# Kernel optimization log

Measured on AMD Instinct MI355X. Metric: run time of the kernel, lower is better.

The kernel has to match this reference:

```python
import jax, jax.numpy as jnp
import numpy as np

B, N, D = 4, 2048, 1024
H = 16
HD = D // H


def setup_inputs() -> dict:
    key = jax.random.key(0)
    ks = jax.random.split(key, 6)
    x = jax.random.normal(ks[0], (B, N, D), dtype=jnp.float32)
    # additive causal mask: 0 on/below diagonal, -inf above
    neg = jnp.float32(-1e9)
    causal_mask = jnp.where(jnp.triu(jnp.ones((N, N), dtype=bool), k=1), neg, 0.0).astype(jnp.float32)
    s = 1.0 / np.sqrt(D)
    Wqkv = jax.random.normal(ks[1], (D, 3 * D), dtype=jnp.float32) * s
    bqkv = jax.random.normal(ks[2], (3 * D,), dtype=jnp.float32) * 0.01
    Wproj = jax.random.normal(ks[3], (D, D), dtype=jnp.float32) * s
    bproj = jax.random.normal(ks[4], (D,), dtype=jnp.float32) * 0.01
    return {"x": x, "causal_mask": causal_mask, "Wqkv": Wqkv, "bqkv": bqkv, "Wproj": Wproj, "bproj": bproj}


def reference(x, causal_mask, Wqkv, bqkv, Wproj, bproj):
    b, n, d = x.shape
    qkv = x @ Wqkv + bqkv  # [B,N,3D]
    qkv = qkv.reshape(b, n, 3, H, HD).transpose(2, 0, 3, 1, 4)  # [3,B,H,N,HD]
    q, k, v = qkv[0], qkv[1], qkv[2]
    scale = HD ** -0.5
    attn = jnp.einsum('bhqd,bhkd->bhqk', q, k) * scale  # [B,H,N,N]
    attn = attn + causal_mask  # broadcast [N,N] -> [B,H,N,N]
    attn = jax.nn.softmax(attn, axis=-1)
    out = jnp.einsum('bhqk,bhkd->bhqd', attn, v)  # [B,H,N,HD]
    out = out.transpose(0, 2, 1, 3).reshape(b, n, d)
    return out @ Wproj + bproj
```

## Files before the change

### kernel.cpp

```cpp
#include <hip/hip_runtime.h>
#include <hip/hip_bf16.h>

typedef unsigned short u16;
typedef unsigned int u32;
typedef __attribute__((ext_vector_type(8))) short bf16x8;
typedef __attribute__((ext_vector_type(4))) float f32x4;
typedef __attribute__((ext_vector_type(16))) float f32x16;

#define AS1(p) ((const __attribute__((address_space(1))) void*)(p))
#define AS3(p) ((__attribute__((address_space(3))) void*)(p))

#if __has_builtin(__builtin_amdgcn_exp2f)
#define EXP2F(x) __builtin_amdgcn_exp2f(x)
#else
#define EXP2F(x) exp2f(x)
#endif

static __device__ __forceinline__ float b2f(u16 u) {
  union { unsigned int i; float f; } v; v.i = ((unsigned int)u) << 16; return v.f;
}
static __device__ __forceinline__ u16 f2b(float f) {
  union { float f; unsigned int i; } v; v.f = f;
  unsigned int r = v.i + 0x7FFFu + ((v.i >> 16) & 1u);
  return (u16)(r >> 16);
}
static __device__ __forceinline__ u32 cvt_pk_bf16(float lo, float hi) {
  u32 r;
  asm("v_cvt_pk_bf16_f32 %0, %1, %2" : "=v"(r) : "v"(lo), "v"(hi));
  return r;
}
static __device__ __forceinline__ void permswap(u32& a, u32& b) {
  asm("v_permlane32_swap_b32 %0, %1" : "+v"(a), "+v"(b));
}

__global__ __launch_bounds__(256) void cast_f32_bf16(const float* __restrict__ src,
                                                     u16* __restrict__ dst, int n8) {
  int stride = gridDim.x * blockDim.x;
  for (int i = blockIdx.x * blockDim.x + threadIdx.x; i < n8; i += stride) {
    const float4* s = (const float4*)(src + (size_t)i * 8);
    float4 a = s[0], b = s[1];
    bf16x8 o;
    o[0] = (short)f2b(a.x); o[1] = (short)f2b(a.y); o[2] = (short)f2b(a.z); o[3] = (short)f2b(a.w);
    o[4] = (short)f2b(b.x); o[5] = (short)f2b(b.y); o[6] = (short)f2b(b.z); o[7] = (short)f2b(b.w);
    *(bf16x8*)(dst + (size_t)i * 8) = o;
  }
}

__global__ __launch_bounds__(256) void transpose_w(const float* __restrict__ src,
                                                   u16* __restrict__ dst,
                                                   int R, int C) {
  __shared__ float tile[32][33];
  int c0 = blockIdx.x * 32, r0 = blockIdx.y * 32;
  int tx = threadIdx.x, ty = threadIdx.y;
  for (int i = ty; i < 32; i += 8) tile[i][tx] = src[(size_t)(r0 + i) * C + c0 + tx];
  __syncthreads();
  for (int i = ty; i < 32; i += 8) dst[(size_t)(c0 + i) * R + r0 + tx] = f2b(tile[tx][i]);
}

__global__ __launch_bounds__(256) void transpose_v(const u16* __restrict__ qkv,
                                                   u16* __restrict__ VT) {
  const int N = 2048, TD = 3072, D = 1024;
  int bh = blockIdx.y, n0 = blockIdx.x * 64;
  int b = bh >> 4, h = bh & 15;
  int tid = threadIdx.x;
  __shared__ u16 tl[64][72];
  #pragma unroll
  for (int i = 0; i < 16; ++i) {
    int idx = tid + i * 256;
    int nl = idx >> 6, dd = idx & 63;
    tl[dd][nl] = qkv[(size_t)(b * N + n0 + nl) * TD + 2 * D + h * 64 + dd];
  }
  __syncthreads();
  #pragma unroll
  for (int i = 0; i < 16; ++i) {
    int idx = tid + i * 256;
    int dd = idx >> 6, nl = idx & 63;
    VT[((size_t)bh * 64 + dd) * N + n0 + nl] = tl[dd][nl];
  }
}

template <typename OutT>
__global__ __launch_bounds__(256) void gemm_bt_bias(
    const u16* __restrict__ A,
    const u16* __restrict__ BT,
    const float* __restrict__ bias,
    OutT* __restrict__ C,
    int M, int N, int K) {
  __shared__ alignas(16) u16 Als[128 * 32];
  __shared__ alignas(16) u16 Bls[128 * 32];
  const int m0 = blockIdx.x * 128, n0 = blockIdx.y * 128;
  const int t = threadIdx.x;
  const int w = t >> 6, lane = t & 63;
  const int wr = w >> 1, wc = w & 1;
  const int rlo = lane & 15, g = lane >> 4;

  f32x4 acc[4][4] = {};

  const int r0 = t >> 2;
  const int c0 = (t & 3) << 3;
  const u16* aSrc = A + (size_t)(m0 + r0) * K + c0;
  const u16* bSrc = BT + (size_t)(n0 + r0) * K + c0;

  for (int k0 = 0; k0 < K; k0 += 32) {
    __builtin_amdgcn_global_load_lds(AS1(aSrc + k0), AS3(&Als[t * 8]), 16, 0, 0);
    __builtin_amdgcn_global_load_lds(AS1(aSrc + (size_t)64 * K + k0), AS3(&Als[(t + 256) * 8]), 16, 0, 0);
    __builtin_amdgcn_global_load_lds(AS1(bSrc + k0), AS3(&Bls[t * 8]), 16, 0, 0);
    __builtin_amdgcn_global_load_lds(AS1(bSrc + (size_t)64 * K + k0), AS3(&Bls[(t + 256) * 8]), 16, 0, 0);
    __syncthreads();

    bf16x8 a[4], b[4];
    #pragma unroll
    for (int m = 0; m < 4; ++m)
      a[m] = *(const bf16x8*)&Als[(wr * 64 + m * 16 + rlo) * 32 + g * 8];
    #pragma unroll
    for (int n = 0; n < 4; ++n)
      b[n] = *(const bf16x8*)&Bls[(wc * 64 + n * 16 + rlo) * 32 + g * 8];
    #pragma unroll
    for (int m = 0; m < 4; ++m)
      #pragma unroll
      for (int n = 0; n < 4; ++n)
        acc[m][n] = __builtin_amdgcn_mfma_f32_16x16x32_bf16(a[m], b[n], acc[m][n], 0, 0, 0);
    __syncthreads();
  }

  #pragma unroll
  for (int n = 0; n < 4; ++n) {
    const int col = n0 + wc * 64 + n * 16 + rlo;
    const float bv = bias[col];
    #pragma unroll
    for (int m = 0; m < 4; ++m) {
      const int row = m0 + wr * 64 + m * 16 + g * 4;
      #pragma unroll
      for (int i = 0; i < 4; ++i) {
        float r = acc[m][n][i] + bv;
        if constexpr (sizeof(OutT) == 2)
          C[(size_t)(row + i) * N + col] = (OutT)f2b(r);
        else
          C[(size_t)(row + i) * N + col] = (OutT)r;
      }
    }
  }
}

__global__ __launch_bounds__(256) void attn_fwd(
    const u16* __restrict__ qkv,
    const u16* __restrict__ VT,
    u16* __restrict__ O) {
  const int N = 2048, TD = 3072, D = 1024;
  const int bid = blockIdx.x;
  const int qp = bid >> 6, bh = bid & 63;
  const int b = bh >> 4, h = bh & 15;
  const int t = threadIdx.x, w = t >> 6, lane = t & 63;
  const int l31 = lane & 31, hi = lane >> 5;

  __shared__ alignas(16) u16 Kls[64 * 64];
  __shared__ alignas(16) u16 Vls[64 * 64];

  const int c1 = t, c2 = t + 256;
  const int r1 = c1 >> 3, sc1 = ((c1 & 7) ^ (r1 & 7)) * 8;
  const int r2 = c2 >> 3, sc2 = ((c2 & 7) ^ (r2 & 7)) * 8;
  const u16* kbase = qkv + (size_t)(b * N) * TD + D + h * 64;
  const u16* vbase = VT + (size_t)bh * 64 * N;

  const float L2E = 1.44269504089f;
  const float NSH = -23.0830992f;

  for (int pass = 0; pass < 2; ++pass) {
    const int qt = pass ? (15 - qp) : qp;
    const int qbase = qt * 128 + w * 32;

    bf16x8 qf[4];
    {
      const u16* qp_ = qkv + ((size_t)(b * N) + qbase + l31) * TD + h * 64 + hi * 8;
      #pragma unroll
      for (int c = 0; c < 4; ++c) {
        bf16x8 v = *(const bf16x8*)(qp_ + c * 16);
        #pragma unroll
        for (int j = 0; j < 8; ++j)
          v[j] = (short)f2b(b2f((u16)v[j]) * 0.125f);
        qf[c] = v;
      }
    }

    f32x16 o_acc[2] = {};
    float psum = 0.f;
    const int jend = qt * 128 + 64;

    for (int j0 = 0; j0 <= jend; j0 += 64) {
      __builtin_amdgcn_global_load_lds(AS1(kbase + (size_t)(j0 + r1) * TD + sc1), AS3(&Kls[c1 * 8]), 16, 0, 0);
      __builtin_amdgcn_global_load_lds(AS1(kbase + (size_t)(j0 + r2) * TD + sc2), AS3(&Kls[c2 * 8]), 16, 0, 0);
      __builtin_amdgcn_global_load_lds(AS1(vbase + (size_t)r1 * N + j0 + sc1), AS3(&Vls[c1 * 8]), 16, 0, 0);
      __builtin_amdgcn_global_load_lds(AS1(vbase + (size_t)r2 * N + j0 + sc2), AS3(&Vls[c2 * 8]), 16, 0, 0);
      __syncthreads();

      if (j0 <= qbase + 31) {
        bf16x8 kf[2][4];
        #pragma unroll
        for (int st = 0; st < 2; ++st) {
          const int row = st * 32 + l31, sw = (row & 7) << 3;
          #pragma unroll
          for (int c = 0; c < 4; ++c)
            kf[st][c] = *(const bf16x8*)&Kls[row * 64 + ((c * 16 + hi * 8) ^ sw)];
        }
        bf16x8 vf[2][2][2];
        #pragma unroll
        for (int dt = 0; dt < 2; ++dt) {
          const int row = dt * 32 + l31, sw = (row & 7) << 3;
          #pragma unroll
          for (int st = 0; st < 2; ++st)
            #pragma unroll
            for (int kc = 0; kc < 2; ++kc)
              vf[st][kc][dt] = *(const bf16x8*)&Vls[row * 64 + ((st * 32 + kc * 16 + hi * 8) ^ sw)];
        }

        const int qr = qbase + l31;
        const bool straddle = !(j0 + 63 <= qbase);
        #pragma unroll
        for (int st = 0; st < 2; ++st) {
          if (st == 1 && !(j0 < qbase)) continue;
          f32x16 S = {};
          __builtin_amdgcn_s_setprio(1);
          #pragma unroll
          for (int c = 0; c < 4; ++c)
            S = __builtin_amdgcn_mfma_f32_32x32x16_bf16(kf[st][c], qf[c], S, 0, 0, 0);
          __builtin_amdgcn_s_setprio(0);
          if (straddle) {
            const int kvb = j0 + st * 32 + 4 * hi;
            #pragma unroll
            for (int r = 0; r < 16; ++r)
              if (kvb + (r & 3) + 8 * (r >> 2) > qr) S[r] = -1e30f;
          }
          float p[16];
          #pragma unroll
          for (int r = 0; r < 16; ++r) p[r] = EXP2F(fmaf(S[r], L2E, NSH));
          float ps = 0.f;
          #pragma unroll
          for (int r = 0; r < 16; ++r) ps += p[r];
          psum += ps;
          u32 wq[8];
          #pragma unroll
          for (int i = 0; i < 8; ++i) wq[i] = cvt_pk_bf16(p[2 * i], p[2 * i + 1]);
          permswap(wq[0], wq[2]); permswap(wq[1], wq[3]);
          permswap(wq[4], wq[6]); permswap(wq[5], wq[7]);
          union { u32 u[4]; bf16x8 v; } pa0, pa1;
          pa0.u[0] = wq[0]; pa0.u[1] = wq[1]; pa0.u[2] = wq[2]; pa0.u[3] = wq[3];
          pa1.u[0] = wq[4]; pa1.u[1] = wq[5]; pa1.u[2] = wq[6]; pa1.u[3] = wq[7];
          __builtin_amdgcn_s_setprio(1);
          #pragma unroll
          for (int dt = 0; dt < 2; ++dt) {
            o_acc[dt] = __builtin_amdgcn_mfma_f32_32x32x16_bf16(pa0.v, vf[st][0][dt], o_acc[dt], 0, 0, 0);
            o_acc[dt] = __builtin_amdgcn_mfma_f32_32x32x16_bf16(pa1.v, vf[st][1][dt], o_acc[dt], 0, 0, 0);
          }
          __builtin_amdgcn_s_setprio(0);
        }
      }
      __syncthreads();
    }

    float rs = psum + __shfl_xor(psum, 32, 64);
    float inv = 1.0f / rs;
    #pragma unroll
    for (int r = 0; r < 16; ++r) {
      const int qrow = (r & 3) + 8 * (r >> 2) + 4 * hi;
      const float invq = __shfl(inv, qrow, 64);
      const int q = qbase + qrow;
      #pragma unroll
      for (int dt = 0; dt < 2; ++dt)
        O[((size_t)(b * N) + q) * D + h * 64 + dt * 32 + l31] = f2b(o_acc[dt][r] * invq);
    }
  }
}

extern "C" void kernel_launch(void* const* d_in, const int* in_sizes, int n_in,
                              void* d_out, int out_size, void* d_ws, size_t ws_size,
                              hipStream_t stream) {
  const float* x     = (const float*)d_in[0];
  const float* Wqkv  = (const float*)d_in[2];
  const float* bqkv  = (const float*)d_in[3];
  const float* Wproj = (const float*)d_in[4];
  const float* bproj = (const float*)d_in[5];
  float* out = (float*)d_out;

  const int B = 4, N = 2048, D = 1024, H = 16;
  const int BN = B * N;
  const int TD = 3 * D;

  char* ws = (char*)d_ws;
  u16* qkv    = (u16*)(ws);
  u16* vt     = (u16*)(ws + 50331648);
  u16* aout   = (u16*)(ws + 67108864);
  u16* wqkvT  = (u16*)(ws + 83886080);
  u16* wprojT = (u16*)(ws + 90177536);
  u16* xb     = (u16*)(ws + 92274688);

  cast_f32_bf16<<<2048, 256, 0, stream>>>(x, xb, BN * D / 8);
  transpose_w<<<dim3(TD / 32, D / 32), dim3(32, 8), 0, stream>>>(Wqkv, wqkvT, D, TD);
  transpose_w<<<dim3(D / 32, D / 32), dim3(32, 8), 0, stream>>>(Wproj, wprojT, D, D);
  gemm_bt_bias<u16><<<dim3(BN / 128, TD / 128), 256, 0, stream>>>(xb, wqkvT, bqkv, qkv, BN, TD, D);
  transpose_v<<<dim3(N / 64, B * H), 256, 0, stream>>>(qkv, vt);
  attn_fwd<<<512, 256, 0, stream>>>(qkv, vt, aout);
  gemm_bt_bias<float><<<dim3(BN / 128, D / 128), 256, 0, stream>>>(aout, wprojT, bproj, out, BN, D, D);
}
```

Before: 194.5 us.

## Replace 128x128 GEMM with double-buffered 256x256 tile kernel using swizzled LDS

Both projection GEMMs move to a new kernel with 256x256 output tiles, 512 threads and a K-step of 64. The next K-tile is prefetched into a second LDS buffer while the current one is being multiplied. The LDS layout is XOR-swizzled to cut bank conflicts, and block IDs are remapped for better L2 locality. MFMA sections raise wave priority, which is meant to raise arithmetic intensity and hide load latency. In exchange, the kernel uses about 128KB of LDS per block, which limits occupancy, and the proj GEMM launches only 128 workgroups.

Result: slower. 216.2 us (+11.2%).

```diff
diff --git a/kernel.cpp b/kernel.cpp
--- a/kernel.cpp
+++ b/kernel.cpp
@@ -9,6 +9,7 @@
 
 #define AS1(p) ((const __attribute__((address_space(1))) void*)(p))
 #define AS3(p) ((__attribute__((address_space(3))) void*)(p))
+#define STG(src, dst) __builtin_amdgcn_global_load_lds(AS1(src), AS3(dst), 16, 0, 0)
 
 #if __has_builtin(__builtin_amdgcn_exp2f)
 #define EXP2F(x) __builtin_amdgcn_exp2f(x)
@@ -80,59 +81,106 @@
 }
 
 template <typename OutT>
-__global__ __launch_bounds__(256) void gemm_bt_bias(
+__global__ __launch_bounds__(512, 2) void gemm256(
     const u16* __restrict__ A,
     const u16* __restrict__ BT,
     const float* __restrict__ bias,
     OutT* __restrict__ C,
-    int M, int N, int K) {
-  __shared__ alignas(16) u16 Als[128 * 32];
-  __shared__ alignas(16) u16 Bls[128 * 32];
-  const int m0 = blockIdx.x * 128, n0 = blockIdx.y * 128;
+    int M, int N, int K, int nm) {
+  __shared__ alignas(16) u16 As[2][2][128 * 64];
+  __shared__ alignas(16) u16 Bs[2][2][128 * 64];
+
+  const int nwg = gridDim.x;
+  const int cpx = nwg >> 3;
+  const int id0 = blockIdx.x;
+  const int swz = (id0 & 7) * cpx + (id0 >> 3);
+  const int mi = swz % nm, ni = swz / nm;
+  const int m0 = mi * 256, n0 = ni * 256;
+
   const int t = threadIdx.x;
-  const int w = t >> 6, lane = t & 63;
-  const int wr = w >> 1, wc = w & 1;
+  const int wid = t >> 6, lane = t & 63;
+  const int wr = wid >> 2, wc = wid & 3;
   const int rlo = lane & 15, g = lane >> 4;
 
-  f32x4 acc[4][4] = {};
-
-  const int r0 = t >> 2;
-  const int c0 = (t & 3) << 3;
-  const u16* aSrc = A + (size_t)(m0 + r0) * K + c0;
-  const u16* bSrc = BT + (size_t)(n0 + r0) * K + c0;
-
-  for (int k0 = 0; k0 < K; k0 += 32) {
-    __builtin_amdgcn_global_load_lds(AS1(aSrc + k0), AS3(&Als[t * 8]), 16, 0, 0);
-    __builtin_amdgcn_global_load_lds(AS1(aSrc + (size_t)64 * K + k0), AS3(&Als[(t + 256) * 8]), 16, 0, 0);
-    __builtin_amdgcn_global_load_lds(AS1(bSrc + k0), AS3(&Bls[t * 8]), 16, 0, 0);
-    __builtin_amdgcn_global_load_lds(AS1(bSrc + (size_t)64 * K + k0), AS3(&Bls[(t + 256) * 8]), 16, 0, 0);
+  const int cs = t ^ (((t >> 5) & 1) << 1);
+  const int sr = cs >> 3, sco = (cs & 7) * 8;
+  const u16* aS0 = A + (size_t)(m0 + sr) * K + sco;
+  const u16* aS1 = A + (size_t)(m0 + 128 + sr) * K + sco;
+  const u16* bS0 = BT + (size_t)(n0 + sr) * K + sco;
+  const u16* bS1 = BT + (size_t)(n0 + 128 + sr) * K + sco;
+  const size_t rowK64 = (size_t)64 * K;
+
+  f32x4 acc[8][4] = {};
+  const int swb = (rlo & 4) ? 32 : 0;
+  const int NT = K >> 6;
+
+  STG(aS0, &As[0][0][t * 8]); STG(aS0 + rowK64, &As[0][0][(t + 512) * 8]);
+  STG(aS1, &As[0][1][t * 8]); STG(aS1 + rowK64, &As[0][1][(t + 512) * 8]);
+  STG(bS0, &Bs[0][0][t * 8]); STG(bS0 + rowK64, &Bs[0][0][(t + 512) * 8]);
+  STG(bS1, &Bs[0][1][t * 8]); STG(bS1 + rowK64, &Bs[0][1][(t + 512) * 8]);
+
+  for (int kt = 0; kt < NT; ++kt) {
+    const int db = kt & 1;
     __syncthreads();
 
-    bf16x8 a[4], b[4];
-    #pragma unroll
-    for (int m = 0; m < 4; ++m)
-      a[m] = *(const bf16x8*)&Als[(wr * 64 + m * 16 + rlo) * 32 + g * 8];
-    #pragma unroll
-    for (int n = 0; n < 4; ++n)
-      b[n] = *(const bf16x8*)&Bls[(wc * 64 + n * 16 + rlo) * 32 + g * 8];
-    #pragma unroll
-    for (int m = 0; m < 4; ++m)
-      #pragma unroll
-      for (int n = 0; n < 4; ++n)
-        acc[m][n] = __builtin_amdgcn_mfma_f32_16x16x32_bf16(a[m], b[n], acc[m][n], 0, 0, 0);
-    __syncthreads();
+    if (kt + 1 < NT) {
+      const int nx = db ^ 1;
+      const size_t ko = (size_t)(kt + 1) * 64;
+      STG(aS0 + ko, &As[nx][0][t * 8]); STG(aS0 + ko + rowK64, &As[nx][0][(t + 512) * 8]);
+      STG(aS1 + ko, &As[nx][1][t * 8]); STG(aS1 + ko + rowK64, &As[nx][1][(t + 512) * 8]);
+      STG(bS0 + ko, &Bs[nx][0][t * 8]); STG(bS0 + ko + rowK64, &Bs[nx][0][(t + 512) * 8]);
+      STG(bS1 + ko, &Bs[nx][1][t * 8]); STG(bS1 + ko + rowK64, &Bs[nx][1][(t + 512) * 8]);
+    }
+
+    const char* aB = (const char*)&As[db][wr][0];
+    const char* bB = (const char*)&Bs[db][wc >> 1][0];
+    const int bRow = (wc & 1) * 64;
+
+    bf16x8 a[4][2], b[2][2];
+#define RDA(mh)                                                          \
+    _Pragma("unroll") for (int fr = 0; fr < 4; ++fr)                     \
+      _Pragma("unroll") for (int kc = 0; kc < 2; ++kc) {                 \
+        const int r_ = (mh) * 64 + fr * 16 + rlo;                        \
+        const int off_ = ((r_ * 64 + kc * 32 + g * 8) * 2) ^ swb;        \
+        a[fr][kc] = *(const bf16x8*)(aB + off_);                         \
+      }
+#define RDB(nh)                                                          \
+    _Pragma("unroll") for (int fn = 0; fn < 2; ++fn)                     \
+      _Pragma("unroll") for (int kc = 0; kc < 2; ++kc) {                 \
+        const int r_ = bRow + (nh) * 32 + fn * 16 + rlo;                 \
+        const int off_ = ((r_ * 64 + kc * 32 + g * 8) * 2) ^ swb;        \
+        b[fn][kc] = *(const bf16x8*)(bB + off_);                         \
+      }
+#define MM(mh, nh)                                                       \
+    __builtin_amdgcn_s_setprio(1);                                       \
+    _Pragma("unroll") for (int fr = 0; fr < 4; ++fr)                     \
+      _Pragma("unroll") for (int fn = 0; fn < 2; ++fn) {                 \
+        f32x4 acv = acc[(mh) * 4 + fr][(nh) * 2 + fn];                   \
+        acv = __builtin_amdgcn_mfma_f32_16x16x32_bf16(a[fr][0], b[fn][0], acv, 0, 0, 0); \
+        acv = __builtin_amdgcn_mfma_f32_16x16x32_bf16(a[fr][1], b[fn][1], acv, 0, 0, 0); \
+        acc[(mh) * 4 + fr][(nh) * 2 + fn] = acv;                         \
+      }                                                                  \
+    __builtin_amdgcn_s_setprio(0);
+
+    RDA(0); RDB(0); MM(0, 0);
+    RDB(1);         MM(0, 1);
+    RDA(1);         MM(1, 1);
+    RDB(0);         MM(1, 0);
+#undef RDA
+#undef RDB
+#undef MM
   }
 
   #pragma unroll
-  for (int n = 0; n < 4; ++n) {
-    const int col = n0 + wc * 64 + n * 16 + rlo;
+  for (int nr = 0; nr < 4; ++nr) {
+    const int col = n0 + wc * 64 + nr * 16 + rlo;
     const float bv = bias[col];
     #pragma unroll
-    for (int m = 0; m < 4; ++m) {
-      const int row = m0 + wr * 64 + m * 16 + g * 4;
+    for (int mr = 0; mr < 8; ++mr) {
+      const int row = m0 + wr * 128 + mr * 16 + g * 4;
       #pragma unroll
       for (int i = 0; i < 4; ++i) {
-        float r = acc[m][n][i] + bv;
+        float r = acc[mr][nr][i] + bv;
         if constexpr (sizeof(OutT) == 2)
           C[(size_t)(row + i) * N + col] = (OutT)f2b(r);
         else
@@ -187,10 +235,10 @@
     const int jend = qt * 128 + 64;
 
     for (int j0 = 0; j0 <= jend; j0 += 64) {
-      __builtin_amdgcn_global_load_lds(AS1(kbase + (size_t)(j0 + r1) * TD + sc1), AS3(&Kls[c1 * 8]), 16, 0, 0);
-      __builtin_amdgcn_global_load_lds(AS1(kbase + (size_t)(j0 + r2) * TD + sc2), AS3(&Kls[c2 * 8]), 16, 0, 0);
-      __builtin_amdgcn_global_load_lds(AS1(vbase + (size_t)r1 * N + j0 + sc1), AS3(&Vls[c1 * 8]), 16, 0, 0);
-      __builtin_amdgcn_global_load_lds(AS1(vbase + (size_t)r2 * N + j0 + sc2), AS3(&Vls[c2 * 8]), 16, 0, 0);
+      STG(kbase + (size_t)(j0 + r1) * TD + sc1, &Kls[c1 * 8]);
+      STG(kbase + (size_t)(j0 + r2) * TD + sc2, &Kls[c2 * 8]);
+      STG(vbase + (size_t)r1 * N + j0 + sc1, &Vls[c1 * 8]);
+      STG(vbase + (size_t)r2 * N + j0 + sc2, &Vls[c2 * 8]);
       __syncthreads();
 
       if (j0 <= qbase + 31) {
@@ -296,8 +344,8 @@
   cast_f32_bf16<<<2048, 256, 0, stream>>>(x, xb, BN * D / 8);
   transpose_w<<<dim3(TD / 32, D / 32), dim3(32, 8), 0, stream>>>(Wqkv, wqkvT, D, TD);
   transpose_w<<<dim3(D / 32, D / 32), dim3(32, 8), 0, stream>>>(Wproj, wprojT, D, D);
-  gemm_bt_bias<u16><<<dim3(BN / 128, TD / 128), 256, 0, stream>>>(xb, wqkvT, bqkv, qkv, BN, TD, D);
+  gemm256<u16><<<384, 512, 0, stream>>>(xb, wqkvT, bqkv, qkv, BN, TD, D, 32);
   transpose_v<<<dim3(N / 64, B * H), 256, 0, stream>>>(qkv, vt);
   attn_fwd<<<512, 256, 0, stream>>>(qkv, vt, aout);
-  gemm_bt_bias<float><<<dim3(BN / 128, D / 128), 256, 0, stream>>>(aout, wprojT, bproj, out, BN, D, D);
-}
+  gemm256<float><<<128, 512, 0, stream>>>(aout, wprojT, bproj, out, BN, D, D, 32);
+}
```

## Rewrite GEMM with 256x128 tiles, LDS double buffering, swizzle and XCD remap

Applied to the files above, without the earlier changes.

Replaces the 128x128 single-buffered GEMM with a 256x128 tile that gives each wave an 8x4 MFMA fragment grid. It double-buffers the LDS stage so the next K-slice loads while the current one is computed, and XOR-swizzles the LDS layout to reduce bank conflicts. It also remaps block IDs across the 8 XCDs for better L2 locality and raises MFMA issue priority. The cost is more registers and LDS per block, and fewer blocks for the projection GEMM (256), which could underfill the CUs.

Measured after the change: 203.2 us. 4.5% more time.

```diff
diff --git a/kernel.cpp b/kernel.cpp
--- a/kernel.cpp
+++ b/kernel.cpp
@@ -9,6 +9,7 @@
 
 #define AS1(p) ((const __attribute__((address_space(1))) void*)(p))
 #define AS3(p) ((__attribute__((address_space(3))) void*)(p))
+#define STG(src, dst) __builtin_amdgcn_global_load_lds(AS1(src), AS3(dst), 16, 0, 0)
 
 #if __has_builtin(__builtin_amdgcn_exp2f)
 #define EXP2F(x) __builtin_amdgcn_exp2f(x)
@@ -80,59 +81,93 @@
 }
 
 template <typename OutT>
-__global__ __launch_bounds__(256) void gemm_bt_bias(
+__global__ __launch_bounds__(256, 2) void gemm256(
     const u16* __restrict__ A,
     const u16* __restrict__ BT,
     const float* __restrict__ bias,
     OutT* __restrict__ C,
-    int M, int N, int K) {
-  __shared__ alignas(16) u16 Als[128 * 32];
-  __shared__ alignas(16) u16 Bls[128 * 32];
-  const int m0 = blockIdx.x * 128, n0 = blockIdx.y * 128;
+    int M, int N, int K, int nn) {
+  __shared__ alignas(16) u16 As[2][256 * 32];
+  __shared__ alignas(16) u16 Bs[2][128 * 32];
+
+  const int nwg = gridDim.x, cpx = nwg >> 3, id0 = blockIdx.x;
+  const int swz = (id0 & 7) * cpx + (id0 >> 3);
+  const int mi = swz / nn, ni = swz % nn;
+  const int m0 = mi * 256, n0 = ni * 128;
+
   const int t = threadIdx.x;
-  const int w = t >> 6, lane = t & 63;
-  const int wr = w >> 1, wc = w & 1;
+  const int wid = t >> 6, lane = t & 63;
+  const int wr = wid >> 1, wc = wid & 1;
   const int rlo = lane & 15, g = lane >> 4;
 
-  f32x4 acc[4][4] = {};
-
-  const int r0 = t >> 2;
-  const int c0 = (t & 3) << 3;
-  const u16* aSrc = A + (size_t)(m0 + r0) * K + c0;
-  const u16* bSrc = BT + (size_t)(n0 + r0) * K + c0;
-
-  for (int k0 = 0; k0 < K; k0 += 32) {
-    __builtin_amdgcn_global_load_lds(AS1(aSrc + k0), AS3(&Als[t * 8]), 16, 0, 0);
-    __builtin_amdgcn_global_load_lds(AS1(aSrc + (size_t)64 * K + k0), AS3(&Als[(t + 256) * 8]), 16, 0, 0);
-    __builtin_amdgcn_global_load_lds(AS1(bSrc + k0), AS3(&Bls[t * 8]), 16, 0, 0);
-    __builtin_amdgcn_global_load_lds(AS1(bSrc + (size_t)64 * K + k0), AS3(&Bls[(t + 256) * 8]), 16, 0, 0);
+  const u16* aSrc[4];
+  const u16* bSrc[2];
+  int dA[4], dB[2];
+  #pragma unroll
+  for (int k = 0; k < 4; ++k) {
+    const int c = t + 256 * k, cs = c ^ ((c >> 3) & 3);
+    aSrc[k] = A + (size_t)(m0 + (cs >> 2)) * K + (cs & 3) * 8;
+    dA[k] = c * 8;
+  }
+  #pragma unroll
+  for (int k = 0; k < 2; ++k) {
+    const int c = t + 256 * k, cs = c ^ ((c >> 3) & 3);
+    bSrc[k] = BT + (size_t)(n0 + (cs >> 2)) * K + (cs & 3) * 8;
+    dB[k] = c * 8;
+  }
+
+  f32x4 acc[8][4] = {};
+  const int NT = K >> 5;
+
+  #pragma unroll
+  for (int k = 0; k < 4; ++k) STG(aSrc[k], &As[0][dA[k]]);
+  #pragma unroll
+  for (int k = 0; k < 2; ++k) STG(bSrc[k], &Bs[0][dB[k]]);
+
+  for (int kt = 0; kt < NT; ++kt) {
+    const int db = kt & 1;
     __syncthreads();
 
-    bf16x8 a[4], b[4];
-    #pragma unroll
-    for (int m = 0; m < 4; ++m)
-      a[m] = *(const bf16x8*)&Als[(wr * 64 + m * 16 + rlo) * 32 + g * 8];
-    #pragma unroll
-    for (int n = 0; n < 4; ++n)
-      b[n] = *(const bf16x8*)&Bls[(wc * 64 + n * 16 + rlo) * 32 + g * 8];
-    #pragma unroll
-    for (int m = 0; m < 4; ++m)
-      #pragma unroll
-      for (int n = 0; n < 4; ++n)
-        acc[m][n] = __builtin_amdgcn_mfma_f32_16x16x32_bf16(a[m], b[n], acc[m][n], 0, 0, 0);
-    __syncthreads();
-  }
-
-  #pragma unroll
-  for (int n = 0; n < 4; ++n) {
-    const int col = n0 + wc * 64 + n * 16 + rlo;
+    if (kt + 1 < NT) {
+      const int nx = db ^ 1, ko = (kt + 1) * 32;
+      #pragma unroll
+      for (int k = 0; k < 4; ++k) STG(aSrc[k] + ko, &As[nx][dA[k]]);
+      #pragma unroll
+      for (int k = 0; k < 2; ++k) STG(bSrc[k] + ko, &Bs[nx][dB[k]]);
+    }
+
+    const char* aB = (const char*)&As[db][0];
+    const char* bB = (const char*)&Bs[db][0];
+    bf16x8 a[8], b[4];
+    #pragma unroll
+    for (int fr = 0; fr < 8; ++fr) {
+      const int r_ = wr * 128 + fr * 16 + rlo;
+      a[fr] = *(const bf16x8*)(aB + (r_ * 64 + ((g ^ ((r_ >> 1) & 3)) << 4)));
+    }
+    #pragma unroll
+    for (int fn = 0; fn < 4; ++fn) {
+      const int r_ = wc * 64 + fn * 16 + rlo;
+      b[fn] = *(const bf16x8*)(bB + (r_ * 64 + ((g ^ ((r_ >> 1) & 3)) << 4)));
+    }
+    __builtin_amdgcn_s_setprio(1);
+    #pragma unroll
+    for (int fr = 0; fr < 8; ++fr)
+      #pragma unroll
+      for (int fn = 0; fn < 4; ++fn)
+        acc[fr][fn] = __builtin_amdgcn_mfma_f32_16x16x32_bf16(a[fr], b[fn], acc[fr][fn], 0, 0, 0);
+    __builtin_amdgcn_s_setprio(0);
+  }
+
+  #pragma unroll
+  for (int fn = 0; fn < 4; ++fn) {
+    const int col = n0 + wc * 64 + fn * 16 + rlo;
     const float bv = bias[col];
     #pragma unroll
-    for (int m = 0; m < 4; ++m) {
-      const int row = m0 + wr * 64 + m * 16 + g * 4;
+    for (int fr = 0; fr < 8; ++fr) {
+      const int row = m0 + wr * 128 + fr * 16 + g * 4;
       #pragma unroll
       for (int i = 0; i < 4; ++i) {
-        float r = acc[m][n][i] + bv;
+        float r = acc[fr][fn][i] + bv;
         if constexpr (sizeof(OutT) == 2)
           C[(size_t)(row + i) * N + col] = (OutT)f2b(r);
         else
@@ -187,10 +222,10 @@
     const int jend = qt * 128 + 64;
 
     for (int j0 = 0; j0 <= jend; j0 += 64) {
-      __builtin_amdgcn_global_load_lds(AS1(kbase + (size_t)(j0 + r1) * TD + sc1), AS3(&Kls[c1 * 8]), 16, 0, 0);
-      __builtin_amdgcn_global_load_lds(AS1(kbase + (size_t)(j0 + r2) * TD + sc2), AS3(&Kls[c2 * 8]), 16, 0, 0);
-      __builtin_amdgcn_global_load_lds(AS1(vbase + (size_t)r1 * N + j0 + sc1), AS3(&Vls[c1 * 8]), 16, 0, 0);
-      __builtin_amdgcn_global_load_lds(AS1(vbase + (size_t)r2 * N + j0 + sc2), AS3(&Vls[c2 * 8]), 16, 0, 0);
+      STG(kbase + (size_t)(j0 + r1) * TD + sc1, &Kls[c1 * 8]);
+      STG(kbase + (size_t)(j0 + r2) * TD + sc2, &Kls[c2 * 8]);
+      STG(vbase + (size_t)r1 * N + j0 + sc1, &Vls[c1 * 8]);
+      STG(vbase + (size_t)r2 * N + j0 + sc2, &Vls[c2 * 8]);
       __syncthreads();
 
       if (j0 <= qbase + 31) {
@@ -296,8 +331,8 @@
   cast_f32_bf16<<<2048, 256, 0, stream>>>(x, xb, BN * D / 8);
   transpose_w<<<dim3(TD / 32, D / 32), dim3(32, 8), 0, stream>>>(Wqkv, wqkvT, D, TD);
   transpose_w<<<dim3(D / 32, D / 32), dim3(32, 8), 0, stream>>>(Wproj, wprojT, D, D);
-  gemm_bt_bias<u16><<<dim3(BN / 128, TD / 128), 256, 0, stream>>>(xb, wqkvT, bqkv, qkv, BN, TD, D);
+  gemm256<u16><<<768, 256, 0, stream>>>(xb, wqkvT, bqkv, qkv, BN, TD, D, 24);
   transpose_v<<<dim3(N / 64, B * H), 256, 0, stream>>>(qkv, vt);
   attn_fwd<<<512, 256, 0, stream>>>(qkv, vt, aout);
-  gemm_bt_bias<float><<<dim3(BN / 128, D / 128), 256, 0, stream>>>(aout, wprojT, bproj, out, BN, D, D);
-}
+  gemm256<float><<<256, 256, 0, stream>>>(aout, wprojT, bproj, out, BN, D, D, 8);
+}
```

## Double-buffer K/V tiles and split KV sub-tiles across waves in attention

Applied to the files above, without the earlier changes.

The K/V LDS staging becomes double-buffered, so the next 64-key tile loads while the current one is computed, which removes one barrier per iteration. Work is also repartitioned: each wave now handles 64 query rows and one 32-key half of every tile, instead of 32 query rows and both halves. Partial outputs and row sums are then combined across wave pairs through LDS at the end. Launch bounds now request two blocks per CU. The cost is double the LDS footprint, more accumulator registers, and an extra cross-wave reduction with added barriers.

Result: faster. 185.9 us (-4.4%).

```diff
diff --git a/kernel.cpp b/kernel.cpp
--- a/kernel.cpp
+++ b/kernel.cpp
@@ -9,6 +9,7 @@
 
 #define AS1(p) ((const __attribute__((address_space(1))) void*)(p))
 #define AS3(p) ((__attribute__((address_space(3))) void*)(p))
+#define STG(src, dst) __builtin_amdgcn_global_load_lds(AS1(src), AS3(dst), 16, 0, 0)
 
 #if __has_builtin(__builtin_amdgcn_exp2f)
 #define EXP2F(x) __builtin_amdgcn_exp2f(x)
@@ -142,7 +143,7 @@
   }
 }
 
-__global__ __launch_bounds__(256) void attn_fwd(
+__global__ __launch_bounds__(256, 2) void attn_fwd(
     const u16* __restrict__ qkv,
     const u16* __restrict__ VT,
     u16* __restrict__ O) {
@@ -152,9 +153,11 @@
   const int b = bh >> 4, h = bh & 15;
   const int t = threadIdx.x, w = t >> 6, lane = t & 63;
   const int l31 = lane & 31, hi = lane >> 5;
-
-  __shared__ alignas(16) u16 Kls[64 * 64];
-  __shared__ alignas(16) u16 Vls[64 * 64];
+  const int qh = w >> 1, st = w & 1;
+
+  __shared__ alignas(16) u16 pool16[2][2][64 * 64];
+  __shared__ float rsLds[2][32];
+  float* poolf = (float*)&pool16[0][0][0];
 
   const int c1 = t, c2 = t + 256;
   const int r1 = c1 >> 3, sc1 = ((c1 & 7) ^ (r1 & 7)) * 8;
@@ -162,70 +165,74 @@
   const u16* kbase = qkv + (size_t)(b * N) * TD + D + h * 64;
   const u16* vbase = VT + (size_t)bh * 64 * N;
 
+#define ASTAGE(buf, j0) do { \
+    STG(kbase + (size_t)((j0) + r1) * TD + sc1, &pool16[buf][0][c1 * 8]); \
+    STG(kbase + (size_t)((j0) + r2) * TD + sc2, &pool16[buf][0][c2 * 8]); \
+    STG(vbase + (size_t)r1 * N + (j0) + sc1, &pool16[buf][1][c1 * 8]); \
+    STG(vbase + (size_t)r2 * N + (j0) + sc2, &pool16[buf][1][c2 * 8]); } while (0)
+
   const float L2E = 1.44269504089f;
   const float NSH = -23.0830992f;
 
   for (int pass = 0; pass < 2; ++pass) {
     const int qt = pass ? (15 - qp) : qp;
-    const int qbase = qt * 128 + w * 32;
-
-    bf16x8 qf[4];
-    {
-      const u16* qp_ = qkv + ((size_t)(b * N) + qbase + l31) * TD + h * 64 + hi * 8;
+    const int qbw = qt * 128 + qh * 64;
+
+    bf16x8 qf[2][4];
+    #pragma unroll
+    for (int qs = 0; qs < 2; ++qs) {
+      const u16* qp_ = qkv + ((size_t)(b * N) + qbw + qs * 32 + l31) * TD + h * 64 + hi * 8;
       #pragma unroll
       for (int c = 0; c < 4; ++c) {
         bf16x8 v = *(const bf16x8*)(qp_ + c * 16);
         #pragma unroll
         for (int j = 0; j < 8; ++j)
           v[j] = (short)f2b(b2f((u16)v[j]) * 0.125f);
-        qf[c] = v;
+        qf[qs][c] = v;
       }
     }
 
-    f32x16 o_acc[2] = {};
-    float psum = 0.f;
+    f32x16 o_acc[2][2] = {};
+    float psum[2] = {0.f, 0.f};
     const int jend = qt * 128 + 64;
 
+    ASTAGE(0, 0);
+    __syncthreads();
+
+    int cur = 0;
     for (int j0 = 0; j0 <= jend; j0 += 64) {
-      __builtin_amdgcn_global_load_lds(AS1(kbase + (size_t)(j0 + r1) * TD + sc1), AS3(&Kls[c1 * 8]), 16, 0, 0);
-      __builtin_amdgcn_global_load_lds(AS1(kbase + (size_t)(j0 + r2) * TD + sc2), AS3(&Kls[c2 * 8]), 16, 0, 0);
-      __builtin_amdgcn_global_load_lds(AS1(vbase + (size_t)r1 * N + j0 + sc1), AS3(&Vls[c1 * 8]), 16, 0, 0);
-      __builtin_amdgcn_global_load_lds(AS1(vbase + (size_t)r2 * N + j0 + sc2), AS3(&Vls[c2 * 8]), 16, 0, 0);
-      __syncthreads();
-
-      if (j0 <= qbase + 31) {
-        bf16x8 kf[2][4];
-        #pragma unroll
-        for (int st = 0; st < 2; ++st) {
+      if (j0 + 64 <= jend) ASTAGE(cur ^ 1, j0 + 64);
+
+      const int sb2 = j0 + st * 32;
+      if (sb2 <= qbw + 63) {
+        bf16x8 kf[4];
+        {
           const int row = st * 32 + l31, sw = (row & 7) << 3;
           #pragma unroll
           for (int c = 0; c < 4; ++c)
-            kf[st][c] = *(const bf16x8*)&Kls[row * 64 + ((c * 16 + hi * 8) ^ sw)];
+            kf[c] = *(const bf16x8*)&pool16[cur][0][row * 64 + ((c * 16 + hi * 8) ^ sw)];
         }
-        bf16x8 vf[2][2][2];
+        bf16x8 vf[2][2];
         #pragma unroll
         for (int dt = 0; dt < 2; ++dt) {
           const int row = dt * 32 + l31, sw = (row & 7) << 3;
           #pragma unroll
-          for (int st = 0; st < 2; ++st)
-            #pragma unroll
-            for (int kc = 0; kc < 2; ++kc)
-              vf[st][kc][dt] = *(const bf16x8*)&Vls[row * 64 + ((st * 32 + kc * 16 + hi * 8) ^ sw)];
+          for (int kc = 0; kc < 2; ++kc)
+            vf[kc][dt] = *(const bf16x8*)&pool16[cur][1][row * 64 + ((st * 32 + kc * 16 + hi * 8) ^ sw)];
         }
 
-        const int qr = qbase + l31;
-        const bool straddle = !(j0 + 63 <= qbase);
-        #pragma unroll
-        for (int st = 0; st < 2; ++st) {
-          if (st == 1 && !(j0 < qbase)) continue;
+        #pragma unroll
+        for (int qs = 0; qs < 2; ++qs) {
+          if (qs == 0 && sb2 > qbw + 31) continue;
+          const int qr = qbw + qs * 32 + l31;
           f32x16 S = {};
           __builtin_amdgcn_s_setprio(1);
           #pragma unroll
           for (int c = 0; c < 4; ++c)
-            S = __builtin_amdgcn_mfma_f32_32x32x16_bf16(kf[st][c], qf[c], S, 0, 0, 0);
+            S = __builtin_amdgcn_mfma_f32_32x32x16_bf16(kf[c], qf[qs][c], S, 0, 0, 0);
           __builtin_amdgcn_s_setprio(0);
-          if (straddle) {
-            const int kvb = j0 + st * 32 + 4 * hi;
+          if (sb2 + 31 > qbw + qs * 32) {
+            const int kvb = sb2 + 4 * hi;
             #pragma unroll
             for (int r = 0; r < 16; ++r)
               if (kvb + (r & 3) + 8 * (r >> 2) > qr) S[r] = -1e30f;
@@ -236,7 +243,7 @@
           float ps = 0.f;
           #pragma unroll
           for (int r = 0; r < 16; ++r) ps += p[r];
-          psum += ps;
+          psum[qs] += ps;
           u32 wq[8];
           #pragma unroll
           for (int i = 0; i < 8; ++i) wq[i] = cvt_pk_bf16(p[2 * i], p[2 * i + 1]);
@@ -248,27 +255,50 @@
           __builtin_amdgcn_s_setprio(1);
           #pragma unroll
           for (int dt = 0; dt < 2; ++dt) {
-            o_acc[dt] = __builtin_amdgcn_mfma_f32_32x32x16_bf16(pa0.v, vf[st][0][dt], o_acc[dt], 0, 0, 0);
-            o_acc[dt] = __builtin_amdgcn_mfma_f32_32x32x16_bf16(pa1.v, vf[st][1][dt], o_acc[dt], 0, 0, 0);
+            o_acc[qs][dt] = __builtin_amdgcn_mfma_f32_32x32x16_bf16(pa0.v, vf[0][dt], o_acc[qs][dt], 0, 0, 0);
+            o_acc[qs][dt] = __builtin_amdgcn_mfma_f32_32x32x16_bf16(pa1.v, vf[1][dt], o_acc[qs][dt], 0, 0, 0);
           }
           __builtin_amdgcn_s_setprio(0);
         }
       }
       __syncthreads();
+      cur ^= 1;
     }
 
-    float rs = psum + __shfl_xor(psum, 32, 64);
-    float inv = 1.0f / rs;
-    #pragma unroll
-    for (int r = 0; r < 16; ++r) {
-      const int qrow = (r & 3) + 8 * (r >> 2) + 4 * hi;
-      const float invq = __shfl(inv, qrow, 64);
-      const int q = qbase + qrow;
-      #pragma unroll
-      for (int dt = 0; dt < 2; ++dt)
-        O[((size_t)(b * N) + q) * D + h * 64 + dt * 32 + l31] = f2b(o_acc[dt][r] * invq);
+    float rsown[2];
+    #pragma unroll
+    for (int qs = 0; qs < 2; ++qs)
+      rsown[qs] = psum[qs] + __shfl_xor(psum[qs], 32, 64);
+
+    #pragma unroll
+    for (int qs = 0; qs < 2; ++qs) {
+      if (st != qs) {
+        #pragma unroll
+        for (int dt = 0; dt < 2; ++dt)
+          #pragma unroll
+          for (int r = 0; r < 16; ++r)
+            poolf[qh * 2048 + (dt * 16 + r) * 64 + lane] = o_acc[qs][dt][r];
+        rsLds[qh][l31] = rsown[qs];
+      }
+      __syncthreads();
+      if (st == qs) {
+        const float inv = 1.0f / (rsown[qs] + rsLds[qh][l31]);
+        #pragma unroll
+        for (int r = 0; r < 16; ++r) {
+          const int qrow = (r & 3) + 8 * (r >> 2) + 4 * hi;
+          const float invq = __shfl(inv, qrow, 64);
+          const int q = qbw + qs * 32 + qrow;
+          #pragma unroll
+          for (int dt = 0; dt < 2; ++dt) {
+            const float val = o_acc[qs][dt][r] + poolf[qh * 2048 + (dt * 16 + r) * 64 + lane];
+            O[((size_t)(b * N) + q) * D + h * 64 + dt * 32 + l31] = f2b(val * invq);
+          }
+        }
+      }
+      __syncthreads();
     }
   }
+#undef ASTAGE
 }
 
 extern "C" void kernel_launch(void* const* d_in, const int* in_sizes, int n_in,
```
